# Optimization experiments

Measured on AMD Instinct MI355X. Metric: run time of the kernel, lower is better.

Reference implementation:

```python
import jax, jax.numpy as jnp
import numpy as np

N_CELLS, C_N, K, D_N = 128, 256, 16, 64
G, HS, HM, HMOD, HEADS = 8, 128, 128, 64, 4


def setup_inputs() -> dict:
    key = jax.random.key(0)
    ks = list(jax.random.split(key, 12))
    rng = np.random.default_rng(0)
    # top-K neighbors per neuron within each cell, self excluded, sorted (as in __init__)
    scores = rng.random((N_CELLS, C_N, C_N), dtype=np.float32)
    scores[:, np.arange(C_N), np.arange(C_N)] = -np.inf
    topk = np.argpartition(-scores, K, axis=-1)[..., :K]
    conn_idx = jnp.asarray(np.sort(topk, axis=-1).astype(np.int32))
    cell_to_group = jnp.asarray((np.arange(N_CELLS) % G).astype(np.int32))

    def nrm(k, shape, scale):
        return jax.random.normal(k, shape, dtype=jnp.float32) * scale

    inp = {
        'h': nrm(ks[0], (N_CELLS, C_N, D_N), 1.0),
        'neuron_id': nrm(ks[1], (N_CELLS, C_N, D_N), 0.02),
        'neuron_key': nrm(ks[2], (N_CELLS, C_N, D_N), 0.02),
        'state_w1': nrm(ks[3], (HS, 2 * D_N), (2.0 / (2 * D_N)) ** 0.5),
        'state_b1': jnp.zeros((HS,), jnp.float32),
        'state_gs1': jnp.ones((G, HS), jnp.float32),
        'state_gb1': jnp.zeros((G, HS), jnp.float32),
        'state_w2': nrm(ks[4], (D_N, HS), 0.1 * (2.0 / HS) ** 0.5),
        'state_b2': jnp.zeros((D_N,), jnp.float32),
        'state_gs2': jnp.ones((G, D_N), jnp.float32),
        'state_gb2': jnp.zeros((G, D_N), jnp.float32),
        'msg_w1': nrm(ks[5], (HM, 2 * D_N), (2.0 / (2 * D_N)) ** 0.5),
        'msg_b1': jnp.zeros((HM,), jnp.float32),
        'msg_gs1': jnp.ones((G, HM), jnp.float32),
        'msg_gb1': jnp.zeros((G, HM), jnp.float32),
        'msg_w2': nrm(ks[6], (D_N, HM), 0.1 * (2.0 / HM) ** 0.5),
        'msg_b2': jnp.zeros((D_N,), jnp.float32),
        'msg_gs2': jnp.ones((G, D_N), jnp.float32),
        'msg_gb2': jnp.zeros((G, D_N), jnp.float32),
        'mod_w1': nrm(ks[7], (N_CELLS, D_N, HMOD), (2.0 / D_N) ** 0.5),
        'mod_b1': jnp.zeros((N_CELLS, HMOD), jnp.float32),
        'mod_w2': nrm(ks[8], (N_CELLS, HMOD, D_N), 0.01 * (2.0 / HMOD) ** 0.5),
        'mod_b2': jnp.zeros((N_CELLS, D_N), jnp.float32),
        'conn_idx': conn_idx,
        'cell_to_group': cell_to_group,
    }
    return inp


def reference(h, neuron_id, neuron_key,
              state_w1, state_b1, state_gs1, state_gb1,
              state_w2, state_b2, state_gs2, state_gb2,
              msg_w1, msg_b1, msg_gs1, msg_gb1,
              msg_w2, msg_b2, msg_gs2, msg_gb2,
              mod_w1, mod_b1, mod_w2, mod_b2,
              conn_idx, cell_to_group):
    g = cell_to_group  # [N]
    dh = D_N // HEADS
    gather = jax.vmap(lambda per_cell, idx: per_cell[idx])  # [C,D],[C,K] -> [C,K,D]

    nbr = gather(h, conn_idx)          # [N,C,K,D] neighbor states
    kid = gather(neuron_id, conn_idx)  # [N,C,K,D] neighbor identity vectors

    # multi-head attention weights over the K neighbors
    q = neuron_key.reshape(N_CELLS, C_N, HEADS, dh)
    kk = kid.reshape(N_CELLS, C_N, K, HEADS, dh)
    logits = jnp.einsum('nchd,nckhd->nckh', q, kk) / (dh ** 0.5)
    attn = jax.nn.softmax(logits, axis=2)  # softmax over K

    # per-edge message MLP with per-group gain/bias
    x = jnp.concatenate([nbr, jnp.broadcast_to(h[:, :, None, :], nbr.shape)], axis=-1)  # [N,C,K,2D]
    m1 = jax.nn.gelu(jnp.einsum('nckf,hf->nckh', x, msg_w1) + msg_b1)
    m1 = m1 * msg_gs1[g][:, None, None, :] + msg_gb1[g][:, None, None, :]
    m2 = jnp.einsum('nckh,dh->nckd', m1, msg_w2) + msg_b2
    m2 = m2 * msg_gs2[g][:, None, None, :] + msg_gb2[g][:, None, None, :]

    # attention-weighted aggregation over neighbors
    m2h = m2.reshape(N_CELLS, C_N, K, HEADS, dh)
    agg = jnp.einsum('nckh,nckhd->nchd', attn, m2h).reshape(N_CELLS, C_N, D_N)

    # state-update MLP with per-group gain/bias
    s_in = jnp.concatenate([h, agg], axis=-1)  # [N,C,2D]
    s1 = jax.nn.gelu(jnp.einsum('ncf,hf->nch', s_in, state_w1) + state_b1)
    s1 = s1 * state_gs1[g][:, None, :] + state_gb1[g][:, None, :]
    delta = jnp.einsum('nch,dh->ncd', s1, state_w2) + state_b2
    delta = delta * state_gs2[g][:, None, :] + state_gb2[g][:, None, :]

    # per-cell batched modulation MLP (mod_w1/mod_w2) gating the update
    pooled = h.mean(axis=1)  # [N,D]
    mh = jnp.tanh(jnp.einsum('nd,ndh->nh', pooled, mod_w1) + mod_b1)
    gate = jnp.tanh(jnp.einsum('nh,nho->no', mh, mod_w2) + mod_b2)  # [N,D]

    return h + gate[:, None, :] * delta
```

## Files before the change

### kernel.cpp

```cpp
#include <hip/hip_runtime.h>
#include <hip/hip_bf16.h>

#define N_CELLS 128
#define C_N     256
#define K_NB    16
#define D_N     64
#define G_N     8
#define HS      128
#define HM      128
#define HMOD    64

typedef __bf16 bf16x8 __attribute__((ext_vector_type(8)));
typedef float  f32x4v __attribute__((ext_vector_type(4)));
typedef _Float16 half2_t __attribute__((ext_vector_type(2)));


__device__ __forceinline__ unsigned cvtpk(float lo, float hi) {
    __hip_bfloat162 t = __float22bfloat162_rn(float2{lo, hi});
    return *reinterpret_cast<unsigned*>(&t);
}

__device__ __forceinline__ unsigned short f2bf(float f) {
    return (unsigned short)(cvtpk(f, 0.f) & 0xffffu);
}

__device__ __forceinline__ float bflo(unsigned u) { return __uint_as_float(u << 16); }
__device__ __forceinline__ float bfhi(unsigned u) { return __uint_as_float(u & 0xffff0000u); }

__device__ __forceinline__ half2_t pkrtz(float lo, float hi) {
    return __builtin_bit_cast(half2_t, __builtin_amdgcn_cvt_pkrtz(lo, hi));
}

__device__ __forceinline__ half2_t h2(unsigned u) {
    return __builtin_bit_cast(half2_t, u);
}

__device__ __forceinline__ f32x4v mfma16(uint4 a, uint4 b, f32x4v c) {
    return __builtin_amdgcn_mfma_f32_16x16x32_bf16(
        __builtin_bit_cast(bf16x8, a), __builtin_bit_cast(bf16x8, b), c, 0, 0, 0);
}

__device__ __forceinline__ float gelu_f(float x) {
    float x2 = x * x;
    float u  = x * fmaf(x2, 0.044715f, 1.0f);
    float e  = __expf(1.5957691216057308f * u);
    float r  = __builtin_amdgcn_rcpf(e + 1.0f);
    return x - x * r;
}

__device__ __forceinline__ float sgelu(float x) {
    float e = __expf(-1.702f * x);
    float r = __builtin_amdgcn_rcpf(e + 1.0f);
    return x * r;
}

__device__ __forceinline__ float tanh_fast(float z) {
    float e = __expf(2.0f * z);
    return 1.0f - 2.0f / (e + 1.0f);
}

__device__ __forceinline__ uint4 packf8(const float* p) {
    float4 a = *(const float4*)p, b = *(const float4*)(p + 4);
    return make_uint4(cvtpk(a.x, a.y), cvtpk(a.z, a.w), cvtpk(b.x, b.y), cvtpk(b.z, b.w));
}

__device__ __forceinline__ void load_w2_folded(
    const float* __restrict__ w2, const float* __restrict__ gs1,
    const float* __restrict__ gb1, const float* __restrict__ gs2,
    const float* __restrict__ b2, const float* __restrict__ gb2,
    int g, int lrow, int lgrp, uint4 wf[4][4], float c2[4])
{
    #pragma unroll
    for (int nb2 = 0; nb2 < 4; ++nb2) {
        int d = nb2 * 16 + lrow;
        float gs2d = gs2[g * 64 + d];
        float cgb = 0.0f;
        #pragma unroll
        for (int kf = 0; kf < 4; ++kf) {
            int k0 = kf * 32 + lgrp * 8;
            const float* wp = w2 + d * 128 + k0;
            float4 wa = *(const float4*)wp, wb = *(const float4*)(wp + 4);
            const float* gp = gs1 + g * 128 + k0;
            float4 ga = *(const float4*)gp, gbv = *(const float4*)(gp + 4);
            const float* bp = gb1 + g * 128 + k0;
            float4 ba = *(const float4*)bp, bbv = *(const float4*)(bp + 4);
            cgb += wa.x*ba.x + wa.y*ba.y + wa.z*ba.z + wa.w*ba.w
                 + wb.x*bbv.x + wb.y*bbv.y + wb.z*bbv.z + wb.w*bbv.w;
            wf[nb2][kf] = make_uint4(
                cvtpk(wa.x*ga.x*gs2d,  wa.y*ga.y*gs2d),
                cvtpk(wa.z*ga.z*gs2d,  wa.w*ga.w*gs2d),
                cvtpk(wb.x*gbv.x*gs2d, wb.y*gbv.y*gs2d),
                cvtpk(wb.z*gbv.z*gs2d, wb.w*gbv.w*gs2d));
        }
        cgb += __shfl_xor(cgb, 16);
        cgb += __shfl_xor(cgb, 32);
        c2[nb2] = fmaf(gs2d, cgb + b2[d], gb2[g * 64 + d]);
    }
}


__global__ __launch_bounds__(512, 2) void prep_kernel(
    const float* __restrict__ h, const float* __restrict__ neuron_id,
    const float* __restrict__ neuron_key,
    const float* __restrict__ msg_w1, const float* __restrict__ msg_b1,
    const float* __restrict__ mod_w1, const float* __restrict__ mod_b1,
    const float* __restrict__ mod_w2, const float* __restrict__ mod_b2,
    const int* __restrict__ conn_idx,
    unsigned short* __restrict__ yws, unsigned short* __restrict__ bews,
    unsigned* __restrict__ att2, float* __restrict__ gatep)
{
    __shared__ __align__(16) unsigned short shmem[8][16 * 256];
    int tid = threadIdx.x, bid = blockIdx.x;
    int wave = tid >> 6, lane = tid & 63;
    int lrow = lane & 15, lgrp = lane >> 4;

    if (bid < 256) {
        int n = bid >> 1;
        int c0 = (bid & 1) * 128 + wave * 16;
        unsigned short* ybuf = shmem[wave];

        uint4 bf[2];
        {
            const float* hp = h + ((size_t)n * C_N + (c0 + lrow)) * 64;
            bf[0] = packf8(hp + lgrp * 8);
            bf[1] = packf8(hp + 32 + lgrp * 8);
        }
        for (int nbM = 0; nbM < 16; ++nbM) {
            int o = nbM * 16 + lrow;
            uint4 af[2];
            #pragma unroll
            for (int kf = 0; kf < 2; ++kf) {
                int k = kf * 32 + lgrp * 8;
                const float* wp = (o < 128) ? (msg_w1 + (size_t)o * 128 + k)
                                            : (msg_w1 + (size_t)(o - 128) * 128 + 64 + k);
                af[kf] = packf8(wp);
            }
            f32x4v acc = {0.f, 0.f, 0.f, 0.f};
            acc = mfma16(af[0], bf[0], acc);
            acc = mfma16(af[1], bf[1], acc);
            float4 addv = {0.f, 0.f, 0.f, 0.f};
            if (nbM >= 8) addv = *(const float4*)(msg_b1 + (nbM - 8) * 16 + lgrp * 4);
            uint2 pk = make_uint2(cvtpk(acc[0] + addv.x, acc[1] + addv.y),
                                  cvtpk(acc[2] + addv.z, acc[3] + addv.w));
            int byte = lrow * 512 + ((nbM * 32 + lgrp * 8) ^ ((lrow & 7) << 4));
            *reinterpret_cast<uint2*>(reinterpret_cast<char*>(ybuf) + byte) = pk;
        }
        #pragma unroll
        for (int pass = 0; pass < 8; ++pass) {
            int idx = pass * 64 + lane;
            int row = idx >> 5, col = idx & 31;
            int byte = row * 512 + ((col * 16) ^ ((row & 7) << 4));
            uint4 v = *reinterpret_cast<const uint4*>(
                reinterpret_cast<const char*>(ybuf) + byte);
            size_t rb = (((size_t)n * C_N + c0 + row) * 128) * 2;
            if (col < 16)
                *reinterpret_cast<uint4*>(reinterpret_cast<char*>(yws) + rb + col * 16) = v;
            else
                *reinterpret_cast<uint4*>(reinterpret_cast<char*>(bews) + rb + (col - 16) * 16) = v;
        }
    } else if (bid < 512) {
        int t = lgrp;
        int base = (bid - 256) * 128 + wave * 16;
        for (int i = 0; i < 16; ++i) {
            int gidx = base + i;
            int jv = conn_idx[(size_t)gidx * 16 + lrow];
            const float* kp = neuron_id + ((size_t)(gidx & ~255) + jv) * 64 + t * 16;
            const float* qp = neuron_key + (size_t)gidx * 64 + t * 16;
            float4 k0 = *(const float4*)kp,       k1 = *(const float4*)(kp + 4),
                   k2 = *(const float4*)(kp + 8), k3 = *(const float4*)(kp + 12);
            float4 q0 = *(const float4*)qp,       q1 = *(const float4*)(qp + 4),
                   q2 = *(const float4*)(qp + 8), q3 = *(const float4*)(qp + 12);
            float dt = k0.x*q0.x + k0.y*q0.y + k0.z*q0.z + k0.w*q0.w
                     + k1.x*q1.x + k1.y*q1.y + k1.z*q1.z + k1.w*q1.w
                     + k2.x*q2.x + k2.y*q2.y + k2.z*q2.z + k2.w*q2.w
                     + k3.x*q3.x + k3.y*q3.y + k3.z*q3.z + k3.w*q3.w;
            float lg = dt * 0.25f;
            float mx = lg;
            mx = fmaxf(mx, __shfl_xor(mx, 1));
            mx = fmaxf(mx, __shfl_xor(mx, 2));
            mx = fmaxf(mx, __shfl_xor(mx, 4));
            mx = fmaxf(mx, __shfl_xor(mx, 8));
            float ex = __expf(lg - mx);
            float sm = ex;
            sm += __shfl_xor(sm, 1);
            sm += __shfl_xor(sm, 2);
            sm += __shfl_xor(sm, 4);
            sm += __shfl_xor(sm, 8);
            float av = ex * __builtin_amdgcn_rcpf(sm);
            float avn = __shfl_down(av, 1);
            if ((lrow & 1) == 0) {
                att2[(size_t)gidx * 32 + (lrow >> 1) * 4 + t] =
                    __builtin_bit_cast(unsigned, __builtin_amdgcn_cvt_pkrtz(av, avn));
            }
        }
    } else {
        int n = bid - 512;
        float* red   = reinterpret_cast<float*>(shmem);
        float* pooled = red + 8 * 64;
        float* mh     = pooled + 64;
        int d = lane, part = wave;
        const float* hn = h + (size_t)n * C_N * 64;
        float acc = 0.0f;
        #pragma unroll 4
        for (int i = 0; i < 32; ++i) acc += hn[(part * 32 + i) * 64 + d];
        red[part * 64 + d] = acc;
        __syncthreads();
        if (tid < 64) {
            float s = 0.0f;
            #pragma unroll
            for (int p = 0; p < 8; ++p) s += red[p * 64 + d];
            pooled[d] = s * (1.0f / 256.0f);
        }
        __syncthreads();
        if (tid < 64) {
            float a1 = mod_b1[n * HMOD + d];
            for (int q = 0; q < 64; ++q)
                a1 = fmaf(pooled[q], mod_w1[((size_t)n * 64 + q) * HMOD + d], a1);
            mh[d] = tanh_fast(a1);
        }
        __syncthreads();
        if (tid < 64) {
            float a2 = mod_b2[n * 64 + d];
            for (int q = 0; q < HMOD; ++q)
                a2 = fmaf(mh[q], mod_w2[((size_t)n * HMOD + q) * 64 + d], a2);
            gatep[n * 64 + d] = tanh_fast(a2);
        }
    }
}


__global__ __launch_bounds__(1024)
__attribute__((amdgpu_waves_per_eu(4, 4)))
void edge_kernel(
    const unsigned short* __restrict__ yws, const unsigned short* __restrict__ bews,
    const unsigned* __restrict__ att2, const int* __restrict__ conn_idx,
    const float* __restrict__ msg_w2, const float* __restrict__ msg_gs1,
    const float* __restrict__ msg_gb1, const float* __restrict__ msg_gs2,
    const float* __restrict__ msg_b2, const float* __restrict__ msg_gb2,
    const int* __restrict__ cell_to_group,
    unsigned short* __restrict__ aggws)
{
    __shared__ __align__(16) unsigned yl32[C_N * 64];
    __shared__ __align__(16) unsigned attl[128 * 32];
    __shared__ __align__(16) uint4 w2l[16 * 64];
    __shared__ float mb2cl[64];
    __shared__ __align__(16) unsigned short pbuf_all[16][8 * 128];
    __shared__ __align__(16) unsigned short aggT_all[16][2 * 64];
    int tid = threadIdx.x, bid = blockIdx.x;
    int n = bid >> 1;
    int wave = tid >> 6, lane = tid & 63;
    int lrow = lane & 15, lgrp = lane >> 4;
    int base = n * C_N + (bid & 1) * 128 + wave * 8;

    {
        const uint4* src = (const uint4*)((const char*)yws + (size_t)n * C_N * 256);
        uint4* dst = (uint4*)yl32;
        #pragma unroll
        for (int it = 0; it < 4; ++it) dst[it * 1024 + tid] = src[it * 1024 + tid];
        const uint4* asrc = (const uint4*)(att2 + ((size_t)n * 256 + (bid & 1) * 128) * 32);
        ((uint4*)attl)[tid] = asrc[tid];
    }
    if (wave == 0) {
        uint4 w2f[4][4];
        float mb2c[4];
        int g = cell_to_group[n];
        load_w2_folded(msg_w2, msg_gs1, msg_gb1, msg_gs2, msg_b2, msg_gb2,
                       g, lrow, lgrp, w2f, mb2c);
        #pragma unroll
        for (int t = 0; t < 4; ++t) {
            #pragma unroll
            for (int kf = 0; kf < 4; ++kf)
                w2l[(t * 4 + kf) * 64 + lane] = w2f[t][kf];
            if (lgrp == 0) mb2cl[t * 16 + lrow] = mb2c[t];
        }
    }
    __syncthreads();

    float mb2r0 = mb2cl[lrow], mb2r1 = mb2cl[16 + lrow],
          mb2r2 = mb2cl[32 + lrow], mb2r3 = mb2cl[48 + lrow];
    char* pbuf_b = reinterpret_cast<char*>(pbuf_all[wave]);
    char* aggT_b = reinterpret_cast<char*>(aggT_all[wave]);
    const unsigned* bews32 = (const unsigned*)bews;

    #pragma unroll 1
    for (int pr = 0; pr < 4; ++pr) {
        int gA = base + pr * 2, gB = gA + 1;
        int jvA = conn_idx[(size_t)gA * 16 + lrow];
        int jvB = conn_idx[(size_t)gB * 16 + lrow];
        unsigned bepA = bews32[(size_t)gA * 64 + lane];
        unsigned bepB = bews32[(size_t)gB * 64 + lane];
        float beA0 = bflo(bepA), beA1 = bfhi(bepA);
        float beB0 = bflo(bepB), beB1 = bfhi(bepB);
        int laA = wave * 8 + pr * 2, laB = laA + 1;

        float pA[4][2] = {{0.f,0.f},{0.f,0.f},{0.f,0.f},{0.f,0.f}};
        float pB[4][2] = {{0.f,0.f},{0.f,0.f},{0.f,0.f},{0.f,0.f}};

        #pragma unroll
        for (int kp = 0; kp < 8; ++kp) {
            int jA0 = __builtin_amdgcn_readlane(jvA, 2 * kp);
            int jA1 = __builtin_amdgcn_readlane(jvA, 2 * kp + 1);
            int jB0 = __builtin_amdgcn_readlane(jvB, 2 * kp);
            int jB1 = __builtin_amdgcn_readlane(jvB, 2 * kp + 1);
            unsigned uyA0 = yl32[jA0 * 64 + lane];
            unsigned uyA1 = yl32[jA1 * 64 + lane];
            unsigned uyB0 = yl32[jB0 * 64 + lane];
            unsigned uyB1 = yl32[jB1 * 64 + lane];
            uint4 aqA = *reinterpret_cast<const uint4*>(&attl[laA * 32 + kp * 4]);
            uint4 aqB = *reinterpret_cast<const uint4*>(&attl[laB * 32 + kp * 4]);

            float gA00 = sgelu(bflo(uyA0) + beA0), gA01 = sgelu(bfhi(uyA0) + beA1);
            float gA10 = sgelu(bflo(uyA1) + beA0), gA11 = sgelu(bfhi(uyA1) + beA1);
            float gB00 = sgelu(bflo(uyB0) + beB0), gB01 = sgelu(bfhi(uyB0) + beB1);
            float gB10 = sgelu(bflo(uyB1) + beB0), gB11 = sgelu(bfhi(uyB1) + beB1);
            half2_t GA0 = pkrtz(gA00, gA10);
            half2_t GA1 = pkrtz(gA01, gA11);
            half2_t GB0 = pkrtz(gB00, gB10);
            half2_t GB1 = pkrtz(gB01, gB11);

            half2_t hA, hB;
            hA = h2(aqA.x); hB = h2(aqB.x);
            pA[0][0] = __builtin_amdgcn_fdot2(GA0, hA, pA[0][0], false);
            pA[0][1] = __builtin_amdgcn_fdot2(GA1, hA, pA[0][1], false);
            pB[0][0] = __builtin_amdgcn_fdot2(GB0, hB, pB[0][0], false);
            pB[0][1] = __builtin_amdgcn_fdot2(GB1, hB, pB[0][1], false);
            hA = h2(aqA.y); hB = h2(aqB.y);
            pA[1][0] = __builtin_amdgcn_fdot2(GA0, hA, pA[1][0], false);
            pA[1][1] = __builtin_amdgcn_fdot2(GA1, hA, pA[1][1], false);
            pB[1][0] = __builtin_amdgcn_fdot2(GB0, hB, pB[1][0], false);
            pB[1][1] = __builtin_amdgcn_fdot2(GB1, hB, pB[1][1], false);
            hA = h2(aqA.z); hB = h2(aqB.z);
            pA[2][0] = __builtin_amdgcn_fdot2(GA0, hA, pA[2][0], false);
            pA[2][1] = __builtin_amdgcn_fdot2(GA1, hA, pA[2][1], false);
            pB[2][0] = __builtin_amdgcn_fdot2(GB0, hB, pB[2][0], false);
            pB[2][1] = __builtin_amdgcn_fdot2(GB1, hB, pB[2][1], false);
            hA = h2(aqA.w); hB = h2(aqB.w);
            pA[3][0] = __builtin_amdgcn_fdot2(GA0, hA, pA[3][0], false);
            pA[3][1] = __builtin_amdgcn_fdot2(GA1, hA, pA[3][1], false);
            pB[3][0] = __builtin_amdgcn_fdot2(GB0, hB, pB[3][0], false);
            pB[3][1] = __builtin_amdgcn_fdot2(GB1, hB, pB[3][1], false);
        }

        #pragma unroll
        for (int t = 0; t < 4; ++t) {
            int rowA = t * 2, rowB = rowA + 1;
            *reinterpret_cast<unsigned*>(
                pbuf_b + rowA * 256 + ((lane * 4) ^ ((rowA & 7) << 4))) =
                cvtpk(pA[t][0], pA[t][1]);
            *reinterpret_cast<unsigned*>(
                pbuf_b + rowB * 256 + ((lane * 4) ^ ((rowB & 7) << 4))) =
                cvtpk(pB[t][0], pB[t][1]);
        }

        #pragma unroll
        for (int t = 0; t < 4; ++t) {
            f32x4v acc = {0.f, 0.f, 0.f, 0.f};
            #pragma unroll
            for (int kf = 0; kf < 4; ++kf) {
                int row = t * 2 + (lrow & 1);
                uint4 a = *reinterpret_cast<const uint4*>(
                    pbuf_b + row * 256 + ((kf * 64 + lgrp * 16) ^ ((row & 7) << 4)));
                acc = mfma16(a, w2l[(t * 4 + kf) * 64 + lane], acc);
            }
            if (lgrp == 0) {
                float mb = (t == 0) ? mb2r0 : (t == 1) ? mb2r1 : (t == 2) ? mb2r2 : mb2r3;
                #pragma unroll
                for (int r = 0; r < 2; ++r) {
                    float v = acc[r] + mb;
                    int byte = r * 128 + ((((t * 16 + lrow)) * 2) ^ ((r & 7) << 4));
                    *reinterpret_cast<unsigned short*>(aggT_b + byte) = f2bf(v);
                }
            }
        }
        if (lane < 16) {
            int row = lane >> 3, col = lane & 7;
            int byte = row * 128 + ((col * 16) ^ ((row & 7) << 4));
            uint4 v = *reinterpret_cast<const uint4*>(aggT_b + byte);
            *reinterpret_cast<uint4*>(
                (char*)aggws + (size_t)(gA + row) * 128 + col * 16) = v;
        }
    }
}


__global__ __launch_bounds__(512, 4) void state_kernel(
    const float* __restrict__ h, const unsigned short* __restrict__ aggws,
    const float* __restrict__ gatep,
    const float* __restrict__ state_w1, const float* __restrict__ state_b1,
    const float* __restrict__ state_gs1, const float* __restrict__ state_gb1,
    const float* __restrict__ state_w2, const float* __restrict__ state_b2,
    const float* __restrict__ state_gs2, const float* __restrict__ state_gb2,
    const int* __restrict__ cell_to_group, float* __restrict__ out)
{
    __shared__ __align__(16) unsigned short w1s[128 * 128];
    __shared__ __align__(16) unsigned short s1b_all[8][16 * 128];
    int tid = threadIdx.x, bid = blockIdx.x;
    int n = bid >> 1;
    int g = cell_to_group[n];

    for (int idx = tid; idx < 2048; idx += 512) {
        int row = idx >> 4, ch = idx & 15;
        uint4 p = packf8(state_w1 + (size_t)row * 128 + ch * 8);
        int byte = row * 256 + ((ch * 16) ^ ((row & 7) << 4));
        *reinterpret_cast<uint4*>(reinterpret_cast<char*>(w1s) + byte) = p;
    }
    __syncthreads();

    int wave = tid >> 6, lane = tid & 63;
    int lrow = lane & 15, lgrp = lane >> 4;
    int c0 = (bid & 1) * 128 + wave * 16;
    unsigned short* s1b = s1b_all[wave];

    uint4 sB[4];
    {
        const float* hp = h + ((size_t)n * C_N + c0 + lrow) * 64;
        sB[0] = packf8(hp + lgrp * 8);
        sB[1] = packf8(hp + 32 + lgrp * 8);
        const char* ap = (const char*)aggws + ((size_t)n * C_N + c0 + lrow) * 128;
        sB[2] = *reinterpret_cast<const uint4*>(ap + lgrp * 16);
        sB[3] = *reinterpret_cast<const uint4*>(ap + 64 + lgrp * 16);
    }
    for (int nbM = 0; nbM < 8; ++nbM) {
        uint4 wA[4];
        #pragma unroll
        for (int kf = 0; kf < 4; ++kf)
            wA[kf] = *reinterpret_cast<const uint4*>(
                reinterpret_cast<const char*>(w1s) +
                (nbM * 16 + lrow) * 256 + ((kf * 64 + lgrp * 16) ^ ((lrow & 7) << 4)));
        f32x4v acc = {0.f, 0.f, 0.f, 0.f};
        #pragma unroll
        for (int kf = 0; kf < 4; ++kf) acc = mfma16(wA[kf], sB[kf], acc);
        float4 b1q = *(const float4*)(state_b1 + nbM * 16 + lgrp * 4);
        float g0 = gelu_f(acc[0] + b1q.x), g1 = gelu_f(acc[1] + b1q.y);
        float g2 = gelu_f(acc[2] + b1q.z), g3 = gelu_f(acc[3] + b1q.w);
        uint2 pk = make_uint2(cvtpk(g0, g1), cvtpk(g2, g3));
        int byte = lrow * 256 + ((nbM * 32 + lgrp * 8) ^ ((lrow & 7) << 4));
        *reinterpret_cast<uint2*>(reinterpret_cast<char*>(s1b) + byte) = pk;
    }

    uint4 w2sf[4][4];
    float sb2c[4];
    load_w2_folded(state_w2, state_gs1, state_gb1, state_gs2, state_b2, state_gb2,
                   g, lrow, lgrp, w2sf, sb2c);
    uint4 s1A[4];
    #pragma unroll
    for (int kf = 0; kf < 4; ++kf)
        s1A[kf] = *reinterpret_cast<const uint4*>(
            reinterpret_cast<const char*>(s1b) +
            lrow * 256 + ((kf * 64 + lgrp * 16) ^ ((lrow & 7) << 4)));

    float* dT = reinterpret_cast<float*>(s1b);
    #pragma unroll
    for (int nb2 = 0; nb2 < 4; ++nb2) {
        f32x4v acc = {0.f, 0.f, 0.f, 0.f};
        #pragma unroll
        for (int kf = 0; kf < 4; ++kf) acc = mfma16(s1A[kf], w2sf[nb2][kf], acc);
        #pragma unroll
        for (int r = 0; r < 4; ++r) {
            int c = lgrp * 4 + r;
            int d = nb2 * 16 + lrow;
            int byte = c * 256 + ((d * 4) ^ ((c & 7) << 4));
            *reinterpret_cast<float*>(reinterpret_cast<char*>(dT) + byte) = acc[r] + sb2c[nb2];
        }
    }
    #pragma unroll
    for (int pass = 0; pass < 4; ++pass) {
        int idx = pass * 64 + lane;
        int row = idx >> 4, col = idx & 15;
        int byte = row * 256 + ((col * 16) ^ ((row & 7) << 4));
        float4 dv = *reinterpret_cast<const float4*>(reinterpret_cast<const char*>(dT) + byte);
        size_t off = ((size_t)n * C_N + c0 + row) * 64 + col * 4;
        float4 hv = *(const float4*)(h + off);
        float4 gv = *(const float4*)(gatep + n * 64 + col * 4);
        float4 o;
        o.x = fmaf(gv.x, dv.x, hv.x);
        o.y = fmaf(gv.y, dv.y, hv.y);
        o.z = fmaf(gv.z, dv.z, hv.z);
        o.w = fmaf(gv.w, dv.w, hv.w);
        *(float4*)(out + off) = o;
    }
}


extern "C" void kernel_launch(void* const* d_in, const int* in_sizes, int n_in,
                              void* d_out, int out_size, void* d_ws, size_t ws_size,
                              hipStream_t stream) {
    (void)in_sizes; (void)n_in; (void)out_size; (void)ws_size;
    const float* h          = (const float*)d_in[0];
    const float* neuron_id  = (const float*)d_in[1];
    const float* neuron_key = (const float*)d_in[2];
    const float* state_w1   = (const float*)d_in[3];
    const float* state_b1   = (const float*)d_in[4];
    const float* state_gs1  = (const float*)d_in[5];
    const float* state_gb1  = (const float*)d_in[6];
    const float* state_w2   = (const float*)d_in[7];
    const float* state_b2   = (const float*)d_in[8];
    const float* state_gs2  = (const float*)d_in[9];
    const float* state_gb2  = (const float*)d_in[10];
    const float* msg_w1     = (const float*)d_in[11];
    const float* msg_b1     = (const float*)d_in[12];
    const float* msg_gs1    = (const float*)d_in[13];
    const float* msg_gb1    = (const float*)d_in[14];
    const float* msg_w2     = (const float*)d_in[15];
    const float* msg_b2     = (const float*)d_in[16];
    const float* msg_gs2    = (const float*)d_in[17];
    const float* msg_gb2    = (const float*)d_in[18];
    const float* mod_w1     = (const float*)d_in[19];
    const float* mod_b1     = (const float*)d_in[20];
    const float* mod_w2     = (const float*)d_in[21];
    const float* mod_b2     = (const float*)d_in[22];
    const int*   conn_idx   = (const int*)d_in[23];
    const int*   c2g        = (const int*)d_in[24];

    char* ws = (char*)d_ws;
    float*          gatep = (float*)ws;
    unsigned short* yws   = (unsigned short*)(ws + (32u << 10));
    unsigned short* bews  = (unsigned short*)(ws + (32u << 10) + (8u << 20));
    unsigned*       att2  = (unsigned*)(ws + (32u << 10) + (16u << 20));
    unsigned short* aggws = (unsigned short*)(ws + (32u << 10) + (24u << 20));
    float* outp = (float*)d_out;

    prep_kernel<<<dim3(640), dim3(512), 0, stream>>>(
        h, neuron_id, neuron_key, msg_w1, msg_b1,
        mod_w1, mod_b1, mod_w2, mod_b2, conn_idx,
        yws, bews, att2, gatep);
    edge_kernel<<<dim3(256), dim3(1024), 0, stream>>>(
        yws, bews, att2, conn_idx,
        msg_w2, msg_gs1, msg_gb1, msg_gs2, msg_b2, msg_gb2, c2g, aggws);
    state_kernel<<<dim3(256), dim3(512), 0, stream>>>(
        h, aggws, gatep,
        state_w1, state_b1, state_gs1, state_gb1,
        state_w2, state_b2, state_gs2, state_gb2, c2g, outp);
}
```

Before: 105.2 us.

## Read gathered neighbor rows and attention directly from global memory instead of LDS staging

Drops the LDS staging of the per-cell y tile (64 KB) and attention block, so the edge kernel gathers neighbor rows and attention weights straight from global memory through the cache. This removes the upfront bulk copy and cuts LDS use, which allows more blocks per CU; launch bounds switch from waves_per_eu(4,4) to a min-blocks hint. In exchange, each gather becomes a global load with higher latency, and the data is reused only if it stays in cache.

Result: slower. 170.0 us (+61.5%).

```diff
diff --git a/kernel.cpp b/kernel.cpp
--- a/kernel.cpp
+++ b/kernel.cpp
@@ -229,9 +229,7 @@
 }
 
 
-__global__ __launch_bounds__(1024)
-__attribute__((amdgpu_waves_per_eu(4, 4)))
-void edge_kernel(
+__global__ __launch_bounds__(1024, 8) void edge_kernel(
     const unsigned short* __restrict__ yws, const unsigned short* __restrict__ bews,
     const unsigned* __restrict__ att2, const int* __restrict__ conn_idx,
     const float* __restrict__ msg_w2, const float* __restrict__ msg_gs1,
@@ -240,8 +238,6 @@
     const int* __restrict__ cell_to_group,
     unsigned short* __restrict__ aggws)
 {
-    __shared__ __align__(16) unsigned yl32[C_N * 64];
-    __shared__ __align__(16) unsigned attl[128 * 32];
     __shared__ __align__(16) uint4 w2l[16 * 64];
     __shared__ float mb2cl[64];
     __shared__ __align__(16) unsigned short pbuf_all[16][8 * 128];
@@ -252,14 +248,6 @@
     int lrow = lane & 15, lgrp = lane >> 4;
     int base = n * C_N + (bid & 1) * 128 + wave * 8;
 
-    {
-        const uint4* src = (const uint4*)((const char*)yws + (size_t)n * C_N * 256);
-        uint4* dst = (uint4*)yl32;
-        #pragma unroll
-        for (int it = 0; it < 4; ++it) dst[it * 1024 + tid] = src[it * 1024 + tid];
-        const uint4* asrc = (const uint4*)(att2 + ((size_t)n * 256 + (bid & 1) * 128) * 32);
-        ((uint4*)attl)[tid] = asrc[tid];
-    }
     if (wave == 0) {
         uint4 w2f[4][4];
         float mb2c[4];
@@ -281,6 +269,7 @@
     char* pbuf_b = reinterpret_cast<char*>(pbuf_all[wave]);
     char* aggT_b = reinterpret_cast<char*>(aggT_all[wave]);
     const unsigned* bews32 = (const unsigned*)bews;
+    const char* ycell = (const char*)yws + (size_t)n * C_N * 256;
 
     #pragma unroll 1
     for (int pr = 0; pr < 4; ++pr) {
@@ -291,7 +280,6 @@
         unsigned bepB = bews32[(size_t)gB * 64 + lane];
         float beA0 = bflo(bepA), beA1 = bfhi(bepA);
         float beB0 = bflo(bepB), beB1 = bfhi(bepB);
-        int laA = wave * 8 + pr * 2, laB = laA + 1;
 
         float pA[4][2] = {{0.f,0.f},{0.f,0.f},{0.f,0.f},{0.f,0.f}};
         float pB[4][2] = {{0.f,0.f},{0.f,0.f},{0.f,0.f},{0.f,0.f}};
@@ -302,12 +290,16 @@
             int jA1 = __builtin_amdgcn_readlane(jvA, 2 * kp + 1);
             int jB0 = __builtin_amdgcn_readlane(jvB, 2 * kp);
             int jB1 = __builtin_amdgcn_readlane(jvB, 2 * kp + 1);
-            unsigned uyA0 = yl32[jA0 * 64 + lane];
-            unsigned uyA1 = yl32[jA1 * 64 + lane];
-            unsigned uyB0 = yl32[jB0 * 64 + lane];
-            unsigned uyB1 = yl32[jB1 * 64 + lane];
-            uint4 aqA = *reinterpret_cast<const uint4*>(&attl[laA * 32 + kp * 4]);
-            uint4 aqB = *reinterpret_cast<const uint4*>(&attl[laB * 32 + kp * 4]);
+            unsigned uyA0 = *reinterpret_cast<const unsigned*>(
+                ycell + (size_t)jA0 * 256 + lane * 4);
+            unsigned uyA1 = *reinterpret_cast<const unsigned*>(
+                ycell + (size_t)jA1 * 256 + lane * 4);
+            unsigned uyB0 = *reinterpret_cast<const unsigned*>(
+                ycell + (size_t)jB0 * 256 + lane * 4);
+            unsigned uyB1 = *reinterpret_cast<const unsigned*>(
+                ycell + (size_t)jB1 * 256 + lane * 4);
+            uint4 aqA = *reinterpret_cast<const uint4*>(att2 + (size_t)gA * 32 + kp * 4);
+            uint4 aqB = *reinterpret_cast<const uint4*>(att2 + (size_t)gB * 32 + kp * 4);
 
             float gA00 = sgelu(bflo(uyA0) + beA0), gA01 = sgelu(bfhi(uyA0) + beA1);
             float gA10 = sgelu(bflo(uyA1) + beA0), gA11 = sgelu(bfhi(uyA1) + beA1);
```
